# Kernel tuning notes

Hardware: AMD Instinct MI355X
Metric: run time of the kernel (lower is better)

## Reference

```python
import jax, jax.numpy as jnp
import numpy as np

N = 100000      # nodes
E = 1600000     # edges (avg degree 16)
IN_CH = 128
OUT_CH = 128
MSG_DIM = 16


def setup_inputs() -> dict:
    key = jax.random.key(0)
    ks = jax.random.split(key, 9)
    x = jax.random.normal(ks[0], (N, IN_CH), dtype=jnp.float32)
    edge_index = jax.random.randint(ks[1], (2, E), 0, N, dtype=jnp.int32)
    last_update = jax.random.randint(ks[2], (N,), 0, N, dtype=jnp.int64)
    t = jax.random.uniform(ks[3], (E,), dtype=jnp.float32)
    msg = jax.random.normal(ks[4], (E, MSG_DIM), dtype=jnp.float32)
    # GCNConv weights (glorot-ish scale) and biases
    W1 = jax.random.normal(ks[5], (IN_CH, OUT_CH), dtype=jnp.float32) / np.sqrt(IN_CH)
    b1 = jnp.zeros((OUT_CH,), dtype=jnp.float32)
    W2 = jax.random.normal(ks[6], (OUT_CH, OUT_CH), dtype=jnp.float32) / np.sqrt(OUT_CH)
    b2 = jnp.zeros((OUT_CH,), dtype=jnp.float32)
    return {"x": x, "last_update": last_update, "edge_index": edge_index,
            "t": t, "msg": msg, "W1": W1, "b1": b1, "W2": W2, "b2": b2}


def _gcn_conv(x, W, b, src, dst, deg_inv_sqrt, n):
    """PyG GCNConv: out = D^{-1/2}(A+I)D^{-1/2} (x W) + b.
    src/dst already include self-loops; deg_inv_sqrt precomputed."""
    h = x @ W                                   # [N, out]
    norm = deg_inv_sqrt[src] * deg_inv_sqrt[dst]  # [E+N]
    msgs = h[src] * norm[:, None]               # gather + scale
    out = jax.ops.segment_sum(msgs, dst, num_segments=n)  # scatter-add
    return out + b


def reference(x, last_update, edge_index, t, msg, W1, b1, W2, b2):
    n = x.shape[0]
    loops = jnp.arange(n, dtype=edge_index.dtype)
    src = jnp.concatenate([edge_index[0], loops])
    dst = jnp.concatenate([edge_index[1], loops])
    # symmetric normalization degree: in-degree over dst with self-loops (>=1)
    deg = jnp.zeros((n,), x.dtype).at[dst].add(jnp.ones_like(src, x.dtype))
    deg_inv_sqrt = jax.lax.rsqrt(deg)
    h = _gcn_conv(x, W1, b1, src, dst, deg_inv_sqrt, n)
    h = jax.nn.relu(h)
    out = _gcn_conv(h, W2, b2, src, dst, deg_inv_sqrt, n)
    return out
```

## Files before the change

kernel.cpp:

```cpp
#include <hip/hip_runtime.h>
#include <hip/hip_fp16.h>
#include <stdint.h>

#define NCH 128

using half8  = __attribute__((ext_vector_type(8))) _Float16;
using floatx4 = __attribute__((ext_vector_type(4))) float;


__global__ __launch_bounds__(256) void count_wprep_kernel(const int* __restrict__ dst,
                                                          int* __restrict__ counts, int E,
                                                          const float* __restrict__ W1,
                                                          const float* __restrict__ W2,
                                                          __half* __restrict__ Wt1,
                                                          __half* __restrict__ Wt2) {
    int b = blockIdx.x;
    if (b < 16) {
        const float* W = (b < 8) ? W1 : W2;
        __half* Wt     = (b < 8) ? Wt1 : Wt2;
        int c = (b & 7) * 256 + threadIdx.x;
        int p = c >> 6, lane = c & 63;
        int kc = p >> 3, ct = p & 7;
        int nn = ct * 16 + (lane & 15);
        int kbase = kc * 32 + (lane >> 4) * 8;
        half8 hv;
#pragma unroll
        for (int j = 0; j < 8; ++j)
            hv[j] = (_Float16)W[(size_t)(kbase + j) * NCH + nn];
        *(half8*)(Wt + (size_t)c * 8) = hv;
    } else {
        int i = (b - 16) * 256 + threadIdx.x;
        if (i < E) atomicAdd(&counts[dst[i]], 1);
    }
}

__global__ __launch_bounds__(1024) void scan1_kernel(const int* __restrict__ counts,
                                                     int* __restrict__ incl,
                                                     int* __restrict__ bsums, int n) {
    __shared__ int tmp[1024];
    int i = blockIdx.x * 1024 + threadIdx.x;
    int v = (i < n) ? counts[i] : 0;
    tmp[threadIdx.x] = v;
    __syncthreads();
    for (int off = 1; off < 1024; off <<= 1) {
        int t = (threadIdx.x >= off) ? tmp[threadIdx.x - off] : 0;
        __syncthreads();
        tmp[threadIdx.x] += t;
        __syncthreads();
    }
    if (i < n) incl[i] = tmp[threadIdx.x];
    if (threadIdx.x == 1023) bsums[blockIdx.x] = tmp[1023];
}

__global__ __launch_bounds__(128) void scan2_kernel(int* __restrict__ bsums, int nb) {
    __shared__ int tmp[128];
    int v = (threadIdx.x < nb) ? bsums[threadIdx.x] : 0;
    tmp[threadIdx.x] = v;
    __syncthreads();
    for (int off = 1; off < 128; off <<= 1) {
        int t = (threadIdx.x >= off) ? tmp[threadIdx.x - off] : 0;
        __syncthreads();
        tmp[threadIdx.x] += t;
        __syncthreads();
    }
    if (threadIdx.x < nb) bsums[threadIdx.x] = tmp[threadIdx.x] - v;
}

__global__ __launch_bounds__(256) void offsets_kernel(const int* __restrict__ incl,
                                                      const int* __restrict__ counts,
                                                      const int* __restrict__ bsums,
                                                      int* __restrict__ offsets,
                                                      int* __restrict__ cursor, int n) {
    int i = blockIdx.x * blockDim.x + threadIdx.x;
    if (i < n) {
        int e = incl[i] - counts[i] + bsums[i >> 10];
        offsets[i] = e;
        cursor[i] = e;
    }
}


__global__ __launch_bounds__(256) void fill_gemm_kernel(const float* __restrict__ A,
                                                        const __half* __restrict__ Wt,
                                                        __half* __restrict__ C, int n,
                                                        int gemm_blocks,
                                                        const int* __restrict__ src,
                                                        const int* __restrict__ dst,
                                                        const int* __restrict__ counts,
                                                        int* __restrict__ cursor,
                                                        unsigned int* __restrict__ emeta,
                                                        int E) {
    __shared__ float4 lds[2048];
    int bid = blockIdx.x;
    if (bid >= gemm_blocks) {
        int i = (bid - gemm_blocks) * 256 + threadIdx.x;
        if (i < E) {
            int s = src[i];
            int d = dst[i];
            unsigned int degp1 = (unsigned int)counts[s] + 1u;
            int pos = atomicAdd(&cursor[d], 1);
            emeta[pos] = (unsigned int)s | (degp1 << 17);
        }
        return;
    }
    int t = threadIdx.x;
    for (int i = t; i < 2048; i += 256) lds[i] = ((const float4*)Wt)[i];
    __syncthreads();

    int wave = t >> 6, lane = t & 63;
    int q = lane >> 4, m16 = lane & 15;
    int rowbase = bid * 128 + wave * 32;

    floatx4 acc[2][8];
#pragma unroll
    for (int g = 0; g < 2; ++g)
#pragma unroll
        for (int ct = 0; ct < 8; ++ct) {
            acc[g][ct][0] = 0.f; acc[g][ct][1] = 0.f;
            acc[g][ct][2] = 0.f; acc[g][ct][3] = 0.f;
        }

    const half8* bfr = (const half8*)lds;

    int ra0 = min(rowbase + m16, n - 1);
    int ra1 = min(rowbase + 16 + m16, n - 1);
    const float* pa0 = A + (size_t)ra0 * NCH;
    const float* pa1 = A + (size_t)ra1 * NCH;

#pragma unroll
    for (int kc = 0; kc < 4; ++kc) {
        int ko = kc * 32 + q * 8;
        float4 f0 = *(const float4*)(pa0 + ko);
        float4 f1 = *(const float4*)(pa0 + ko + 4);
        float4 g0 = *(const float4*)(pa1 + ko);
        float4 g1 = *(const float4*)(pa1 + ko + 4);
        half8 a0, a1;
        a0[0] = (_Float16)f0.x; a0[1] = (_Float16)f0.y;
        a0[2] = (_Float16)f0.z; a0[3] = (_Float16)f0.w;
        a0[4] = (_Float16)f1.x; a0[5] = (_Float16)f1.y;
        a0[6] = (_Float16)f1.z; a0[7] = (_Float16)f1.w;
        a1[0] = (_Float16)g0.x; a1[1] = (_Float16)g0.y;
        a1[2] = (_Float16)g0.z; a1[3] = (_Float16)g0.w;
        a1[4] = (_Float16)g1.x; a1[5] = (_Float16)g1.y;
        a1[6] = (_Float16)g1.z; a1[7] = (_Float16)g1.w;
#pragma unroll
        for (int ct = 0; ct < 8; ++ct) {
            half8 b = bfr[(kc * 8 + ct) * 64 + lane];
            acc[0][ct] = __builtin_amdgcn_mfma_f32_16x16x32_f16(a0, b, acc[0][ct], 0, 0, 0);
            acc[1][ct] = __builtin_amdgcn_mfma_f32_16x16x32_f16(a1, b, acc[1][ct], 0, 0, 0);
        }
    }

    __syncthreads();
    float* scr = (float*)lds + wave * 2048;
#pragma unroll
    for (int g = 0; g < 2; ++g) {
#pragma unroll
        for (int reg = 0; reg < 4; ++reg)
#pragma unroll
            for (int ct = 0; ct < 8; ++ct)
                scr[(q * 4 + reg) * NCH + ct * 16 + m16] = acc[g][ct][reg];
        int row0 = rowbase + g * 16;
#pragma unroll
        for (int r = 0; r < 16; ++r) {
            int row = row0 + r;
            if (row < n) {
                float2 v = *(float2*)(scr + r * NCH + lane * 2);
                __half2 hh = __floats2half2_rn(v.x, v.y);
                *(unsigned int*)(C + (size_t)row * NCH + lane * 2) = *(unsigned int*)&hh;
            }
        }
    }
}


__global__ __launch_bounds__(256) void gemm_h_kernel(const __half* __restrict__ A,
                                                     const __half* __restrict__ Wt,
                                                     __half* __restrict__ C, int n) {
    __shared__ float4 lds[2048];
    int t = threadIdx.x;
    for (int i = t; i < 2048; i += 256) lds[i] = ((const float4*)Wt)[i];
    __syncthreads();

    int wave = t >> 6, lane = t & 63;
    int q = lane >> 4, m16 = lane & 15;
    int rowbase = blockIdx.x * 128 + wave * 32;

    floatx4 acc[2][8];
#pragma unroll
    for (int g = 0; g < 2; ++g)
#pragma unroll
        for (int ct = 0; ct < 8; ++ct) {
            acc[g][ct][0] = 0.f; acc[g][ct][1] = 0.f;
            acc[g][ct][2] = 0.f; acc[g][ct][3] = 0.f;
        }

    const half8* bfr = (const half8*)lds;

    int ra0 = min(rowbase + m16, n - 1);
    int ra1 = min(rowbase + 16 + m16, n - 1);
    const _Float16* pa0 = (const _Float16*)A + (size_t)ra0 * NCH;
    const _Float16* pa1 = (const _Float16*)A + (size_t)ra1 * NCH;

#pragma unroll
    for (int kc = 0; kc < 4; ++kc) {
        int ko = kc * 32 + q * 8;
        half8 a0 = *(const half8*)(pa0 + ko);
        half8 a1 = *(const half8*)(pa1 + ko);
#pragma unroll
        for (int ct = 0; ct < 8; ++ct) {
            half8 b = bfr[(kc * 8 + ct) * 64 + lane];
            acc[0][ct] = __builtin_amdgcn_mfma_f32_16x16x32_f16(a0, b, acc[0][ct], 0, 0, 0);
            acc[1][ct] = __builtin_amdgcn_mfma_f32_16x16x32_f16(a1, b, acc[1][ct], 0, 0, 0);
        }
    }

    __syncthreads();
    float* scr = (float*)lds + wave * 2048;
#pragma unroll
    for (int g = 0; g < 2; ++g) {
#pragma unroll
        for (int reg = 0; reg < 4; ++reg)
#pragma unroll
            for (int ct = 0; ct < 8; ++ct)
                scr[(q * 4 + reg) * NCH + ct * 16 + m16] = acc[g][ct][reg];
        int row0 = rowbase + g * 16;
#pragma unroll
        for (int r = 0; r < 16; ++r) {
            int row = row0 + r;
            if (row < n) {
                float2 v = *(float2*)(scr + r * NCH + lane * 2);
                __half2 hh = __floats2half2_rn(v.x, v.y);
                *(unsigned int*)(C + (size_t)row * NCH + lane * 2) = *(unsigned int*)&hh;
            }
        }
    }
}


__global__ __launch_bounds__(256) void agg_kernel(const __half2* __restrict__ hp,
                                                  const int* __restrict__ offsets,
                                                  const int* __restrict__ counts,
                                                  const unsigned int* __restrict__ emeta,
                                                  const float* __restrict__ bias,
                                                  void* __restrict__ outp,
                                                  int n, int do_relu, int out_fp16) {
    int gw = (blockIdx.x * blockDim.x + threadIdx.x) >> 6;
    int lane = threadIdx.x & 63;
    if (gw >= n) return;
    int node = gw;

    int o = offsets[node];
    int c = counts[node];
    float dn = rsqrtf((float)(c + 1));

    float2 hv = __half22float2(hp[(size_t)node * 64 + lane]);
    float w0s = dn * dn;
    float ax = hv.x * w0s, ay = hv.y * w0s;

    unsigned int m = (lane < c) ? emeta[o + lane] : 0u;
    int cc = min(c, 64);
    int j = 0;
    for (; j + 4 <= cc; j += 4) {
        unsigned int p0 = (unsigned int)__shfl((int)m, j);
        unsigned int p1 = (unsigned int)__shfl((int)m, j + 1);
        unsigned int p2 = (unsigned int)__shfl((int)m, j + 2);
        unsigned int p3 = (unsigned int)__shfl((int)m, j + 3);
        int s0 = p0 & 0x1FFFF; float w0 = rsqrtf((float)(p0 >> 17)) * dn;
        int s1 = p1 & 0x1FFFF; float w1 = rsqrtf((float)(p1 >> 17)) * dn;
        int s2 = p2 & 0x1FFFF; float w2 = rsqrtf((float)(p2 >> 17)) * dn;
        int s3 = p3 & 0x1FFFF; float w3 = rsqrtf((float)(p3 >> 17)) * dn;
        float2 v0 = __half22float2(hp[(size_t)s0 * 64 + lane]);
        float2 v1 = __half22float2(hp[(size_t)s1 * 64 + lane]);
        float2 v2 = __half22float2(hp[(size_t)s2 * 64 + lane]);
        float2 v3 = __half22float2(hp[(size_t)s3 * 64 + lane]);
        ax = fmaf(v0.x, w0, ax); ay = fmaf(v0.y, w0, ay);
        ax = fmaf(v1.x, w1, ax); ay = fmaf(v1.y, w1, ay);
        ax = fmaf(v2.x, w2, ax); ay = fmaf(v2.y, w2, ay);
        ax = fmaf(v3.x, w3, ax); ay = fmaf(v3.y, w3, ay);
    }
    for (; j < cc; ++j) {
        unsigned int p = (unsigned int)__shfl((int)m, j);
        int s = p & 0x1FFFF; float w = rsqrtf((float)(p >> 17)) * dn;
        float2 v = __half22float2(hp[(size_t)s * 64 + lane]);
        ax = fmaf(v.x, w, ax); ay = fmaf(v.y, w, ay);
    }
    for (int e = o + 64; e < o + c; ++e) {
        unsigned int p = emeta[e];
        int s = p & 0x1FFFF; float w = rsqrtf((float)(p >> 17)) * dn;
        float2 v = __half22float2(hp[(size_t)s * 64 + lane]);
        ax = fmaf(v.x, w, ax); ay = fmaf(v.y, w, ay);
    }

    float2 b = ((const float2*)bias)[lane];
    ax += b.x;
    ay += b.y;
    if (do_relu) { ax = fmaxf(ax, 0.f); ay = fmaxf(ay, 0.f); }
    if (out_fp16) {
        __half2 hh = __floats2half2_rn(ax, ay);
        ((__half2*)outp)[(size_t)node * 64 + lane] = hh;
    } else {
        float2 o2; o2.x = ax; o2.y = ay;
        ((float2*)outp)[(size_t)node * 64 + lane] = o2;
    }
}


extern "C" void kernel_launch(void* const* d_in, const int* in_sizes, int n_in,
                              void* d_out, int out_size, void* d_ws, size_t ws_size,
                              hipStream_t stream) {
    const float* x  = (const float*)d_in[0];
    const int* edge = (const int*)d_in[2];
    const float* W1 = (const float*)d_in[5];
    const float* b1 = (const float*)d_in[6];
    const float* W2 = (const float*)d_in[7];
    const float* b2 = (const float*)d_in[8];

    int n = in_sizes[0] / NCH;
    int E = in_sizes[2] / 2;
    const int* srcp = edge;
    const int* dstp = edge + E;

    char* ws = (char*)d_ws;
    int*   counts  = (int*)ws;   ws += (size_t)n * 4;
    int*   incl    = (int*)ws;   ws += (size_t)n * 4;
    int*   offsets = (int*)ws;   ws += (size_t)n * 4;
    int*   cursor  = (int*)ws;   ws += (size_t)n * 4;
    int*   bsums   = (int*)ws;   ws += 1024;
    uintptr_t pw = ((uintptr_t)ws + 255) & ~(uintptr_t)255;
    __half* Wt1 = (__half*)pw;   pw += 2048 * 16;
    __half* Wt2 = (__half*)pw;   pw += 2048 * 16;
    unsigned int* emeta = (unsigned int*)pw; pw += (size_t)E * 4;
    uintptr_t p = (pw + 255) & ~(uintptr_t)255;
    __half* h = (__half*)p;
    float* out = (float*)d_out;
    __half* a1 = (__half*)d_out;

    hipMemsetAsync(counts, 0, (size_t)n * 4, stream);

    int count_blocks = (E + 255) / 256;
    count_wprep_kernel<<<16 + count_blocks, 256, 0, stream>>>(dstp, counts, E, W1, W2, Wt1, Wt2);

    int nb = (n + 1023) / 1024;
    scan1_kernel<<<nb, 1024, 0, stream>>>(counts, incl, bsums, n);
    scan2_kernel<<<1, 128, 0, stream>>>(bsums, nb);
    offsets_kernel<<<(n + 255) / 256, 256, 0, stream>>>(incl, counts, bsums, offsets, cursor, n);

    int gemm_blocks = (n + 127) / 128;
    int fill_blocks = (E + 255) / 256;
    int agg_blocks  = (n + 3) / 4;

    fill_gemm_kernel<<<gemm_blocks + fill_blocks, 256, 0, stream>>>(
        x, Wt1, h, n, gemm_blocks, srcp, dstp, counts, cursor, emeta, E);

    agg_kernel<<<agg_blocks, 256, 0, stream>>>((const __half2*)h, offsets, counts, emeta, b1, a1, n, 1, 1);
    gemm_h_kernel<<<gemm_blocks, 256, 0, stream>>>(a1, Wt2, h, n);
    agg_kernel<<<agg_blocks, 256, 0, stream>>>((const __half2*)h, offsets, counts, emeta, b2, out, n, 0, 0);
}
```

Baseline: 487.6 us.

## Partition CSR fill by destination range per XCD with work-stealing chunk queues

```diff
diff --git a/kernel.cpp b/kernel.cpp
--- a/kernel.cpp
+++ b/kernel.cpp
@@ -6,6 +6,7 @@
 
 using half8  = __attribute__((ext_vector_type(8))) _Float16;
 using floatx4 = __attribute__((ext_vector_type(4))) float;
+using intx4  = __attribute__((ext_vector_type(4))) int;
 
 
 __global__ __launch_bounds__(256) void count_wprep_kernel(const int* __restrict__ dst,
@@ -89,25 +90,47 @@
                                                         const int* __restrict__ counts,
                                                         int* __restrict__ cursor,
                                                         unsigned int* __restrict__ emeta,
-                                                        int E) {
+                                                        int E, int* __restrict__ qc,
+                                                        int nch) {
     __shared__ float4 lds[2048];
     int bid = blockIdx.x;
+    int tid = threadIdx.x;
     if (bid >= gemm_blocks) {
-        int i = (bid - gemm_blocks) * 256 + threadIdx.x;
-        if (i < E) {
-            int s = src[i];
-            int d = dst[i];
-            unsigned int degp1 = (unsigned int)counts[s] + 1u;
-            int pos = atomicAdd(&cursor[d], 1);
-            emeta[pos] = (unsigned int)s | (degp1 << 17);
+        int* shq = (int*)lds;
+        int g = __builtin_amdgcn_s_getreg(6164) & 7;
+        for (int pass = 0; pass < 8; ++pass) {
+            int q = (g + pass) & 7;
+            int lo = (int)(((long long)n * q) >> 3);
+            int hi = (int)(((long long)n * (q + 1)) >> 3);
+            for (;;) {
+                __syncthreads();
+                if (tid == 0) shq[0] = atomicAdd(&qc[q], 1);
+                __syncthreads();
+                int c = shq[0];
+                if (c >= nch) break;
+                int i4 = (c << 10) + (tid << 2);
+                if (i4 < E) {
+                    intx4 dv = __builtin_nontemporal_load((const intx4*)(dst + i4));
+                    intx4 sv = __builtin_nontemporal_load((const intx4*)(src + i4));
+#pragma unroll
+                    for (int e = 0; e < 4; ++e) {
+                        int d = dv[e];
+                        if (d >= lo && d < hi) {
+                            int s = sv[e];
+                            unsigned int degp1 = (unsigned int)counts[s] + 1u;
+                            int pos = atomicAdd(&cursor[d], 1);
+                            emeta[pos] = (unsigned int)s | (degp1 << 17);
+                        }
+                    }
+                }
+            }
         }
         return;
     }
-    int t = threadIdx.x;
-    for (int i = t; i < 2048; i += 256) lds[i] = ((const float4*)Wt)[i];
-    __syncthreads();
-
-    int wave = t >> 6, lane = t & 63;
+    for (int i = tid; i < 2048; i += 256) lds[i] = ((const float4*)Wt)[i];
+    __syncthreads();
+
+    int wave = tid >> 6, lane = tid & 63;
     int q = lane >> 4, m16 = lane & 15;
     int rowbase = bid * 128 + wave * 32;
 
@@ -323,6 +346,7 @@
 
     char* ws = (char*)d_ws;
     int*   counts  = (int*)ws;   ws += (size_t)n * 4;
+    int*   qc      = (int*)ws;   ws += 64;
     int*   incl    = (int*)ws;   ws += (size_t)n * 4;
     int*   offsets = (int*)ws;   ws += (size_t)n * 4;
     int*   cursor  = (int*)ws;   ws += (size_t)n * 4;
@@ -336,7 +360,7 @@
     float* out = (float*)d_out;
     __half* a1 = (__half*)d_out;
 
-    hipMemsetAsync(counts, 0, (size_t)n * 4, stream);
+    hipMemsetAsync(counts, 0, (size_t)n * 4 + 64, stream);
 
     int count_blocks = (E + 255) / 256;
     count_wprep_kernel<<<16 + count_blocks, 256, 0, stream>>>(dstp, counts, E, W1, W2, Wt1, Wt2);
@@ -347,11 +371,12 @@
     offsets_kernel<<<(n + 255) / 256, 256, 0, stream>>>(incl, counts, bsums, offsets, cursor, n);
 
     int gemm_blocks = (n + 127) / 128;
-    int fill_blocks = (E + 255) / 256;
+    int fill_blocks = 4096;
+    int nch = (E + 1023) >> 10;
     int agg_blocks  = (n + 3) / 4;
 
     fill_gemm_kernel<<<gemm_blocks + fill_blocks, 256, 0, stream>>>(
-        x, Wt1, h, n, gemm_blocks, srcp, dstp, counts, cursor, emeta, E);
+        x, Wt1, h, n, gemm_blocks, srcp, dstp, counts, cursor, emeta, E, qc, nch);
 
     agg_kernel<<<agg_blocks, 256, 0, stream>>>((const __half2*)h, offsets, counts, emeta, b1, a1, n, 1, 1);
     gemm_h_kernel<<<gemm_blocks, 256, 0, stream>>>(a1, Wt2, h, n);
```

Measured after the change: 933.7 us. 91.5% more time.
